# Kernel optimization log

Measured on AMD Instinct MI355X. Metric: run time of the kernel, lower is better.

## Reference

```python
import jax, jax.numpy as jnp
import numpy as np

N_HEADS = 16


def layernorm(x, g, b, eps=1e-5):
    mu = jnp.mean(x, axis=-1, keepdims=True)
    var = jnp.var(x, axis=-1, keepdims=True)
    return (x - mu) * jax.lax.rsqrt(var + eps) * g + b


def mha(x, w_qkv, b_qkv, w_o, b_o, n_heads):
    # standard multi-head self-attention (dropout off / eval mode)
    B, S, D = x.shape
    hd = D // n_heads
    qkv = x @ w_qkv + b_qkv                      # [B,S,3D]
    q, k, v = jnp.split(qkv, 3, axis=-1)
    q = q.reshape(B, S, n_heads, hd).transpose(0, 2, 1, 3)  # bhsd
    k = k.reshape(B, S, n_heads, hd).transpose(0, 2, 1, 3)
    v = v.reshape(B, S, n_heads, hd).transpose(0, 2, 1, 3)
    att = jnp.einsum('bhqd,bhkd->bhqk', q, k) / jnp.sqrt(jnp.asarray(hd, x.dtype))
    att = jax.nn.softmax(att, axis=-1)
    out = jnp.einsum('bhqk,bhkd->bhqd', att, v)
    out = out.transpose(0, 2, 1, 3).reshape(B, S, D)
    return out @ w_o + b_o


def setup_inputs() -> dict:
    key = jax.random.key(0)
    ks = jax.random.split(key, 12)
    B, Sx, Sz, D = 4, 1024, 1024, 1024
    H = D * 4
    s = 0.02
    return {
        'x': jax.random.normal(ks[0], (B, Sx, D), jnp.float32),
        'z': jax.random.normal(ks[1], (B, Sz, D), jnp.float32),
        'g1': jnp.ones((D,), jnp.float32),
        'b1': jnp.zeros((D,), jnp.float32),
        'w_qkv': jax.random.normal(ks[2], (D, 3 * D), jnp.float32) * s,
        'b_qkv': jnp.zeros((3 * D,), jnp.float32),
        'w_o': jax.random.normal(ks[3], (D, D), jnp.float32) * s,
        'b_o': jnp.zeros((D,), jnp.float32),
        'w_kv': jax.random.normal(ks[4], (D, 2 * D), jnp.float32) * s,
        'b_kv': jnp.zeros((2 * D,), jnp.float32),
        'g2': jnp.ones((D,), jnp.float32),
        'b2': jnp.zeros((D,), jnp.float32),
        'w_m1': jax.random.normal(ks[5], (D, H), jnp.float32) * s,
        'b_m1': jnp.zeros((H,), jnp.float32),
        'w_m2': jax.random.normal(ks[6], (H, D), jnp.float32) * s,
        'b_m2': jnp.zeros((D,), jnp.float32),
    }


def reference(x, z, g1, b1, w_qkv, b_qkv, w_o, b_o, w_kv, b_kv, g2, b2, w_m1, b_m1, w_m2, b_m2):
    # q = x + self_mha(ln1(x))
    q = x + mha(layernorm(x, g1, b1), w_qkv, b_qkv, w_o, b_o, N_HEADS)
    # single-head cross attention: k,v from z, scale by sqrt(dim)
    kv = z @ w_kv + b_kv
    k, v = jnp.split(kv, 2, axis=-1)            # each [B,Sz,D]
    scale = jnp.sqrt(jnp.asarray(k.shape[-1], x.dtype))
    att = jax.nn.softmax(jnp.einsum('bqd,bkd->bqk', q, k) / scale, axis=-1)
    out = jnp.einsum('bqk,bkd->bqd', att, v)
    # out = out + mlp(ln2(out))
    h = layernorm(out, g2, b2)
    h = jax.nn.gelu(h @ w_m1 + b_m1) @ w_m2 + b_m2
    return out + h
```

## Files before the change

kernel.cpp:

```cpp
#include <hip/hip_runtime.h>
#include <cstdint>
#include <cstddef>

using u16 = unsigned short;

typedef __attribute__((ext_vector_type(4))) float f32x4;
typedef __attribute__((ext_vector_type(8))) short bf16x8;

#define DEV static __device__ __forceinline__

DEV float bf2f(u16 v) {
  union { unsigned u; float f; } x; x.u = ((unsigned)v) << 16; return x.f;
}
DEV u16 f2bf(float f) {
  union { float f; unsigned u; } x; x.f = f;
  unsigned r = x.u + 0x7fffu + ((x.u >> 16) & 1u);
  return (u16)(r >> 16);
}
DEV void gload16(const void* g, void* l) {
  __builtin_amdgcn_global_load_lds((const __attribute__((address_space(1))) void*)g,
                                   (__attribute__((address_space(3))) void*)l, 16, 0, 0);
}
DEV float fast_gelu(float x) {
  float y = 0.7978845608028654f * (x + 0.044715f * x * x * x);
  y = fminf(fmaxf(y, -15.0f), 15.0f);
  float e = __expf(2.0f * y);
  float t = (e - 1.0f) / (e + 1.0f);
  return 0.5f * x * (1.0f + t);
}

template <typename OutT, bool GELU, int BN, bool SPLIT>
__global__ __launch_bounds__(256, 2) void gemm_nt(
    const u16* __restrict__ A, const u16* __restrict__ Bt, OutT* __restrict__ C,
    int K, int lda, int ldb, int ldc,
    const float* __restrict__ bias,
    const float* __restrict__ resF, const u16* __restrict__ resB, int ldr,
    float scale,
    long long sA, long long sB, long long sC, long long sR,
    int kSlices)
{
  constexpr int NW = (BN == 128) ? 64 : 32;
  constexpr int NJ = NW / 16;
  __shared__ u16 As[128 * 32];
  __shared__ u16 Bs[BN * 32];

  const int z = blockIdx.z;
  const int bz = z / kSlices;
  const int ks = z - bz * kSlices;
  const int Ksl = K / kSlices;
  const int kbeg = ks * Ksl, kend = kbeg + Ksl;

  A  += (size_t)bz * sA;
  Bt += (size_t)bz * sB;
  if constexpr (SPLIT) C += (size_t)ks * sC;
  else                 C += (size_t)bz * sC;
  const int m0 = blockIdx.y * 128, n0 = blockIdx.x * BN;
  const int tid = threadIdx.x;
  const int lane = tid & 63, wave = tid >> 6;
  const int wm = (wave >> 1) * 64, wn = (wave & 1) * NW;
  const int m15 = lane & 15, quad = lane >> 4;

  const u16* Ab = A + (size_t)m0 * lda;
  const u16* Bb = Bt + (size_t)n0 * ldb;
  const int r0 = tid >> 2, cc8 = (tid & 3) * 8;

  f32x4 acc[4][NJ];
#pragma unroll
  for (int i = 0; i < 4; i++)
#pragma unroll
    for (int j = 0; j < NJ; j++) acc[i][j] = (f32x4){0.f, 0.f, 0.f, 0.f};

  for (int k0 = kbeg; k0 < kend; k0 += 32) {
    __syncthreads();
    gload16(Ab + (size_t)r0 * lda + k0 + cc8,        &As[tid * 8]);
    gload16(Ab + (size_t)(r0 + 64) * lda + k0 + cc8, &As[2048 + tid * 8]);
    gload16(Bb + (size_t)r0 * ldb + k0 + cc8,        &Bs[tid * 8]);
    if constexpr (BN == 128)
      gload16(Bb + (size_t)(r0 + 64) * ldb + k0 + cc8, &Bs[2048 + tid * 8]);
    __syncthreads();
    bf16x8 af[4], bfr[NJ];
#pragma unroll
    for (int i = 0; i < 4; i++) af[i]  = *(const bf16x8*)&As[(wm + i * 16 + m15) * 32 + quad * 8];
#pragma unroll
    for (int j = 0; j < NJ; j++) bfr[j] = *(const bf16x8*)&Bs[(wn + j * 16 + m15) * 32 + quad * 8];
#pragma unroll
    for (int i = 0; i < 4; i++)
#pragma unroll
      for (int j = 0; j < NJ; j++)
        acc[i][j] = __builtin_amdgcn_mfma_f32_16x16x32_bf16(af[i], bfr[j], acc[i][j], 0, 0, 0);
  }

  const float* resFb = resF ? resF + (size_t)bz * sR : nullptr;
  const u16*   resBb = resB ? resB + (size_t)bz * sR : nullptr;

#pragma unroll
  for (int i = 0; i < 4; i++) {
    const int rowb = m0 + wm + i * 16 + quad * 4;
#pragma unroll
    for (int r = 0; r < 4; r++) {
      const size_t rowoff = (size_t)(rowb + r) * ldc;
      const size_t resoff = (size_t)(rowb + r) * ldr;
#pragma unroll
      for (int j = 0; j < NJ; j++) {
        const int col = n0 + wn + j * 16 + m15;
        float v = acc[i][j][r] * scale;
        if constexpr (SPLIT) {
          ((u16*)C)[rowoff + col] = f2bf(v);
        } else {
          if (bias) v += bias[col];
          if (GELU) v = fast_gelu(v);
          if (resFb) v += resFb[resoff + col];
          if (resBb) v += bf2f(resBb[resoff + col]);
          if constexpr (sizeof(OutT) == 4) C[rowoff + col] = v;
          else ((u16*)C)[rowoff + col] = f2bf(v);
        }
      }
    }
  }
}

__global__ __launch_bounds__(256) void mlp2_reduce_k(
    const u16* __restrict__ part, long long sliceStride,
    const u16* __restrict__ outb, const float* __restrict__ b_m2,
    float* __restrict__ outF)
{
  const size_t i = (size_t)blockIdx.x * 256 + threadIdx.x;
  const int col = (int)((i * 4) & 1023);
  const ushort4 u = ((const ushort4*)outb)[i];
  float4 o;
  o.x = bf2f(u.x) + b_m2[col + 0];
  o.y = bf2f(u.y) + b_m2[col + 1];
  o.z = bf2f(u.z) + b_m2[col + 2];
  o.w = bf2f(u.w) + b_m2[col + 3];
#pragma unroll
  for (int ks = 0; ks < 4; ks++) {
    const ushort4 p = ((const ushort4*)(part + (size_t)ks * sliceStride))[i];
    o.x += bf2f(p.x); o.y += bf2f(p.y); o.z += bf2f(p.z); o.w += bf2f(p.w);
  }
  ((float4*)outF)[i] = o;
}

__global__ __launch_bounds__(256) void transpose_all_k(
    const float* __restrict__ w_qkv, const float* __restrict__ w_o,
    const float* __restrict__ w_kv,  const float* __restrict__ w_m1,
    const float* __restrict__ w_m2,
    u16* __restrict__ wqkvT, u16* __restrict__ woT, u16* __restrict__ wkvT,
    u16* __restrict__ wm1T,  u16* __restrict__ wm2T)
{
  __shared__ u16 tile[32][33];
  int idx = blockIdx.x;
  const float* in; u16* out; int gx, ldin, ldout;
  if (idx < 3072)      { in = w_qkv; out = wqkvT; gx = 96;  ldin = 3072; ldout = 1024; }
  else if (idx < 4096) { idx -= 3072; in = w_o;  out = woT;  gx = 32;  ldin = 1024; ldout = 1024; }
  else if (idx < 6144) { idx -= 4096; in = w_kv; out = wkvT; gx = 64;  ldin = 2048; ldout = 1024; }
  else if (idx < 10240){ idx -= 6144; in = w_m1; out = wm1T; gx = 128; ldin = 4096; ldout = 1024; }
  else                 { idx -= 10240; in = w_m2; out = wm2T; gx = 32; ldin = 1024; ldout = 4096; }
  const int bx = idx % gx, by = idx / gx;
  const int tx = threadIdx.x & 31, ty = threadIdx.x >> 5;
  const int x = bx * 32 + tx;
#pragma unroll
  for (int j = 0; j < 4; j++)
    tile[ty + j * 8][tx] = f2bf(in[(size_t)(by * 32 + ty + j * 8) * ldin + x]);
  __syncthreads();
  const int x2 = by * 32 + tx;
#pragma unroll
  for (int j = 0; j < 4; j++)
    out[(size_t)(bx * 32 + ty + j * 8) * ldout + x2] = tile[tx][ty + j * 8];
}

__global__ __launch_bounds__(256) void transpose_v_self(
    const u16* __restrict__ qkv, u16* __restrict__ vT)
{
  __shared__ u16 tile[32][33];
  const int z = blockIdx.z, b = z >> 4, h = z & 15;
  const u16* in = qkv + (size_t)b * 1024 * 3072 + 2048 + h * 64;
  u16* out = vT + (size_t)z * 64 * 1024;
  const int tx = threadIdx.x & 31, ty = threadIdx.x >> 5;
  const int key0 = blockIdx.x * 32, d0 = blockIdx.y * 32;
#pragma unroll
  for (int j = 0; j < 4; j++)
    tile[ty + j * 8][tx] = in[(size_t)(key0 + ty + j * 8) * 3072 + d0 + tx];
  __syncthreads();
#pragma unroll
  for (int j = 0; j < 4; j++)
    out[(size_t)(d0 + ty + j * 8) * 1024 + key0 + tx] = tile[tx][ty + j * 8];
}

__global__ __launch_bounds__(256, 2) void flash_self_attn2(
    const u16* __restrict__ qkv, const u16* __restrict__ vT, u16* __restrict__ outp)
{
  __shared__ u16 Ks[64 * 72];
  __shared__ u16 Vs[64 * 72];
  __shared__ u16 Ps[128 * 72];
  const int b = blockIdx.z, h = blockIdx.y, q0 = blockIdx.x * 128;
  const int tid = threadIdx.x;
  const int lane = tid & 63, w = tid >> 6;
  const int m15 = lane & 15, quad = lane >> 4;

  const size_t base = (size_t)b * 1024 * 3072;
  const u16* qb  = qkv + base + (size_t)q0 * 3072 + h * 64;
  const u16* kb  = qkv + base + 1024 + h * 64;
  const u16* vtb = vT + (size_t)(b * 16 + h) * 64 * 1024;

  const int r8 = tid >> 3, c8 = (tid & 7) * 8;

  bf16x8 aq[2][2];
#pragma unroll
  for (int rb = 0; rb < 2; rb++)
#pragma unroll
    for (int kk = 0; kk < 2; kk++)
      aq[rb][kk] = *(const bf16x8*)(qb + (size_t)(w * 32 + rb * 16 + m15) * 3072 + kk * 32 + quad * 8);

  float m_i[2][4], l_i[2][4];
  f32x4 oacc[2][4];
#pragma unroll
  for (int rb = 0; rb < 2; rb++) {
#pragma unroll
    for (int r = 0; r < 4; r++) { m_i[rb][r] = -1e30f; l_i[rb][r] = 0.f; }
#pragma unroll
    for (int d = 0; d < 4; d++) oacc[rb][d] = (f32x4){0.f, 0.f, 0.f, 0.f};
  }

  for (int kt = 0; kt < 16; kt++) {
    const int key0 = kt * 64;
    bf16x8 kreg[2], vreg[2];
#pragma unroll
    for (int i = 0; i < 2; i++) {
      kreg[i] = *(const bf16x8*)(kb + (size_t)(key0 + r8 + i * 32) * 3072 + c8);
      vreg[i] = *(const bf16x8*)(vtb + (size_t)(r8 + i * 32) * 1024 + key0 + c8);
    }
    __syncthreads();
#pragma unroll
    for (int i = 0; i < 2; i++) {
      *(bf16x8*)&Ks[(r8 + i * 32) * 72 + c8] = kreg[i];
      *(bf16x8*)&Vs[(r8 + i * 32) * 72 + c8] = vreg[i];
    }
    __syncthreads();

    f32x4 sacc[2][4];
#pragma unroll
    for (int rb = 0; rb < 2; rb++)
#pragma unroll
      for (int n = 0; n < 4; n++) sacc[rb][n] = (f32x4){0.f, 0.f, 0.f, 0.f};
#pragma unroll
    for (int kk = 0; kk < 2; kk++)
#pragma unroll
      for (int n = 0; n < 4; n++) {
        const bf16x8 bk = *(const bf16x8*)&Ks[(n * 16 + m15) * 72 + kk * 32 + quad * 8];
#pragma unroll
        for (int rb = 0; rb < 2; rb++)
          sacc[rb][n] = __builtin_amdgcn_mfma_f32_16x16x32_bf16(aq[rb][kk], bk, sacc[rb][n], 0, 0, 0);
      }

#pragma unroll
    for (int rb = 0; rb < 2; rb++) {
      float al[4], rs[4];
#pragma unroll
      for (int r = 0; r < 4; r++) {
        float v = fmaxf(fmaxf(sacc[rb][0][r], sacc[rb][1][r]), fmaxf(sacc[rb][2][r], sacc[rb][3][r]));
        v *= 0.125f;
#pragma unroll
        for (int off = 1; off < 16; off <<= 1) v = fmaxf(v, __shfl_xor(v, off));
        const float mnew = fmaxf(m_i[rb][r], v);
        al[r] = __expf(m_i[rb][r] - mnew);
        m_i[rb][r] = mnew;
        rs[r] = 0.f;
      }
#pragma unroll
      for (int n = 0; n < 4; n++)
#pragma unroll
        for (int r = 0; r < 4; r++) {
          const float p = __expf(sacc[rb][n][r] * 0.125f - m_i[rb][r]);
          rs[r] += p;
          Ps[(w * 32 + rb * 16 + quad * 4 + r) * 72 + n * 16 + m15] = f2bf(p);
        }
#pragma unroll
      for (int r = 0; r < 4; r++) {
#pragma unroll
        for (int off = 1; off < 16; off <<= 1) rs[r] += __shfl_xor(rs[r], off);
        l_i[rb][r] = l_i[rb][r] * al[r] + rs[r];
      }
#pragma unroll
      for (int d = 0; d < 4; d++)
#pragma unroll
        for (int r = 0; r < 4; r++) oacc[rb][d][r] *= al[r];
    }

    bf16x8 ap[2][2];
#pragma unroll
    for (int rb = 0; rb < 2; rb++)
#pragma unroll
      for (int kk = 0; kk < 2; kk++)
        ap[rb][kk] = *(const bf16x8*)&Ps[(w * 32 + rb * 16 + m15) * 72 + kk * 32 + quad * 8];
#pragma unroll
    for (int kk = 0; kk < 2; kk++)
#pragma unroll
      for (int d = 0; d < 4; d++) {
        const bf16x8 bv = *(const bf16x8*)&Vs[(d * 16 + m15) * 72 + kk * 32 + quad * 8];
#pragma unroll
        for (int rb = 0; rb < 2; rb++)
          oacc[rb][d] = __builtin_amdgcn_mfma_f32_16x16x32_bf16(ap[rb][kk], bv, oacc[rb][d], 0, 0, 0);
      }
  }

#pragma unroll
  for (int rb = 0; rb < 2; rb++) {
    u16* ob = outp + (size_t)(b * 1024 + q0 + w * 32 + rb * 16 + quad * 4) * 1024 + h * 64 + m15;
#pragma unroll
    for (int r = 0; r < 4; r++) {
      const float inv = 1.0f / l_i[rb][r];
#pragma unroll
      for (int d = 0; d < 4; d++)
        ob[(size_t)r * 1024 + d * 16] = f2bf(oacc[rb][d][r] * inv);
    }
  }
}

template <typename TIn>
__global__ __launch_bounds__(256) void layernorm_k(
    const TIn* __restrict__ x, const float* __restrict__ g, const float* __restrict__ bb,
    u16* __restrict__ y)
{
  const int row = blockIdx.x;
  const int t = threadIdx.x;
  float v[4];
  if constexpr (sizeof(TIn) == 4) {
    const float4 f = ((const float4*)((const float*)x + (size_t)row * 1024))[t];
    v[0] = f.x; v[1] = f.y; v[2] = f.z; v[3] = f.w;
  } else {
    const ushort4 u = ((const ushort4*)((const u16*)x + (size_t)row * 1024))[t];
    v[0] = bf2f(u.x); v[1] = bf2f(u.y); v[2] = bf2f(u.z); v[3] = bf2f(u.w);
  }
  float s = v[0] + v[1] + v[2] + v[3];
  float sq = v[0]*v[0] + v[1]*v[1] + v[2]*v[2] + v[3]*v[3];
#pragma unroll
  for (int off = 1; off < 64; off <<= 1) { s += __shfl_xor(s, off); sq += __shfl_xor(sq, off); }
  __shared__ float red[8];
  const int wv = t >> 6;
  if ((t & 63) == 0) { red[wv] = s; red[4 + wv] = sq; }
  __syncthreads();
  s = red[0] + red[1] + red[2] + red[3];
  sq = red[4] + red[5] + red[6] + red[7];
  const float mean = s * (1.0f / 1024.0f);
  const float var = sq * (1.0f / 1024.0f) - mean * mean;
  const float rstd = rsqrtf(var + 1e-5f);
  const int c = t * 4;
  ushort4 o;
  o.x = f2bf((v[0] - mean) * rstd * g[c + 0] + bb[c + 0]);
  o.y = f2bf((v[1] - mean) * rstd * g[c + 1] + bb[c + 1]);
  o.z = f2bf((v[2] - mean) * rstd * g[c + 2] + bb[c + 2]);
  o.w = f2bf((v[3] - mean) * rstd * g[c + 3] + bb[c + 3]);
  ((ushort4*)(y + (size_t)row * 1024))[t] = o;
}

__global__ __launch_bounds__(256) void softmax_rows_k(const float* __restrict__ S, u16* __restrict__ P)
{
  const int row = blockIdx.x;
  const int t = threadIdx.x;
  const float4 f = ((const float4*)(S + (size_t)row * 1024))[t];
  float mx = fmaxf(fmaxf(f.x, f.y), fmaxf(f.z, f.w));
#pragma unroll
  for (int off = 1; off < 64; off <<= 1) mx = fmaxf(mx, __shfl_xor(mx, off));
  __shared__ float red[8];
  const int wv = t >> 6;
  if ((t & 63) == 0) red[wv] = mx;
  __syncthreads();
  mx = fmaxf(fmaxf(red[0], red[1]), fmaxf(red[2], red[3]));
  float e0 = __expf(f.x - mx), e1 = __expf(f.y - mx), e2 = __expf(f.z - mx), e3 = __expf(f.w - mx);
  float s = e0 + e1 + e2 + e3;
#pragma unroll
  for (int off = 1; off < 64; off <<= 1) s += __shfl_xor(s, off);
  if ((t & 63) == 0) red[4 + wv] = s;
  __syncthreads();
  s = red[4] + red[5] + red[6] + red[7];
  const float inv = 1.0f / s;
  ushort4 o; o.x = f2bf(e0 * inv); o.y = f2bf(e1 * inv); o.z = f2bf(e2 * inv); o.w = f2bf(e3 * inv);
  ((ushort4*)(P + (size_t)row * 1024))[t] = o;
}

__global__ __launch_bounds__(256) void transpose_k(
    const u16* __restrict__ in, u16* __restrict__ out,
    int ldin, int ldout, long long sIn, long long sOut)
{
  __shared__ u16 tile[32][33];
  in  += (size_t)blockIdx.z * sIn;
  out += (size_t)blockIdx.z * sOut;
  const int tx = threadIdx.x & 31, ty = threadIdx.x >> 5;
  const int x = blockIdx.x * 32 + tx;
#pragma unroll
  for (int j = 0; j < 4; j++)
    tile[ty + j * 8][tx] = in[(size_t)(blockIdx.y * 32 + ty + j * 8) * ldin + x];
  __syncthreads();
  const int x2 = blockIdx.y * 32 + tx;
#pragma unroll
  for (int j = 0; j < 4; j++)
    out[(size_t)(blockIdx.x * 32 + ty + j * 8) * ldout + x2] = tile[tx][ty + j * 8];
}

__global__ __launch_bounds__(256) void cast_f2b_k(const float* __restrict__ in, u16* __restrict__ out)
{
  const size_t i = (size_t)blockIdx.x * 256 + threadIdx.x;
  const float4 f = ((const float4*)in)[i];
  ushort4 o; o.x = f2bf(f.x); o.y = f2bf(f.y); o.z = f2bf(f.z); o.w = f2bf(f.w);
  ((ushort4*)out)[i] = o;
}

extern "C" void kernel_launch(void* const* d_in, const int* in_sizes, int n_in,
                              void* d_out, int out_size, void* d_ws, size_t ws_size,
                              hipStream_t stream)
{
  const float* x     = (const float*)d_in[0];
  const float* z     = (const float*)d_in[1];
  const float* g1    = (const float*)d_in[2];
  const float* b1    = (const float*)d_in[3];
  const float* w_qkv = (const float*)d_in[4];
  const float* b_qkv = (const float*)d_in[5];
  const float* w_o   = (const float*)d_in[6];
  const float* b_o   = (const float*)d_in[7];
  const float* w_kv  = (const float*)d_in[8];
  const float* b_kv  = (const float*)d_in[9];
  const float* g2    = (const float*)d_in[10];
  const float* b2    = (const float*)d_in[11];
  const float* w_m1  = (const float*)d_in[12];
  const float* b_m1  = (const float*)d_in[13];
  const float* w_m2  = (const float*)d_in[14];
  const float* b_m2  = (const float*)d_in[15];
  float* outF = (float*)d_out;

  char* ws = (char*)d_ws;
  const size_t MB = 1024ull * 1024ull;
  u16*   qkv   = (u16*)(ws + 0);
  u16*   Pm    = (u16*)(ws + 0);
  u16*   hm    = (u16*)(ws + 0);
  u16*   zb    = (u16*)(ws + 24 * MB);
  u16*   vTs   = (u16*)(ws + 24 * MB);
  u16*   xln   = (u16*)(ws + 32 * MB);
  u16*   mpart = (u16*)(ws + 32 * MB);
  u16*   qbuf  = (u16*)(ws + 40 * MB);
  u16*   kv    = (u16*)(ws + 48 * MB);
  float* Ssc   = (float*)(ws + 64 * MB);
  u16*   h1    = (u16*)(ws + 64 * MB);
  u16*   outb  = (u16*)(ws + 80 * MB);
  u16*   wqkvT = (u16*)(ws + 88 * MB);
  u16*   woT   = (u16*)(ws + 94 * MB);
  u16*   wkvT  = (u16*)(ws + 96 * MB);
  u16*   wm1T  = (u16*)(ws + 100 * MB);
  u16*   wm2T  = (u16*)(ws + 108 * MB);
  u16*   vT    = (u16*)(ws + 116 * MB);

  dim3 blk(256);
  const long long M1 = 1024 * 1024;

  hipLaunchKernelGGL(transpose_all_k, dim3(14336), blk, 0, stream,
                     w_qkv, w_o, w_kv, w_m1, w_m2, wqkvT, woT, wkvT, wm1T, wm2T);

  hipLaunchKernelGGL(cast_f2b_k, dim3(4096), blk, 0, stream, z, zb);
  hipLaunchKernelGGL((layernorm_k<float>), dim3(4096), blk, 0, stream, x, g1, b1, xln);

  hipLaunchKernelGGL((gemm_nt<u16, false, 128, false>), dim3(16, 32, 1), blk, 0, stream,
                     zb, wkvT, kv, 1024, 1024, 1024, 2048,
                     b_kv, (const float*)nullptr, (const u16*)nullptr, 0, 1.0f, 0LL, 0LL, 0LL, 0LL, 1);
  hipLaunchKernelGGL((gemm_nt<u16, false, 128, false>), dim3(24, 32, 1), blk, 0, stream,
                     xln, wqkvT, qkv, 1024, 1024, 1024, 3072,
                     b_qkv, (const float*)nullptr, (const u16*)nullptr, 0, 1.0f, 0LL, 0LL, 0LL, 0LL, 1);
  hipLaunchKernelGGL(transpose_v_self, dim3(32, 2, 64), blk, 0, stream, qkv, vTs);
  hipLaunchKernelGGL(flash_self_attn2, dim3(8, 16, 4), blk, 0, stream, qkv, vTs, xln);
  hipLaunchKernelGGL((gemm_nt<u16, false, 64, false>), dim3(16, 32, 1), blk, 0, stream,
                     xln, woT, qbuf, 1024, 1024, 1024, 1024,
                     b_o, x, (const u16*)nullptr, 1024, 1.0f, 0LL, 0LL, 0LL, 0LL, 1);
  hipLaunchKernelGGL((gemm_nt<float, false, 64, false>), dim3(16, 8, 4), blk, 0, stream,
                     qbuf, kv, Ssc, 1024, 1024, 2048, 1024,
                     (const float*)nullptr, (const float*)nullptr, (const u16*)nullptr, 0,
                     0.03125f, M1, 2 * M1, M1, 0LL, 1);
  hipLaunchKernelGGL(softmax_rows_k, dim3(4096), blk, 0, stream, Ssc, Pm);
  hipLaunchKernelGGL(transpose_k, dim3(32, 32, 4), blk, 0, stream,
                     kv + 1024, vT, 2048, 1024, 2 * M1, M1);
  hipLaunchKernelGGL((gemm_nt<u16, false, 64, false>), dim3(16, 8, 4), blk, 0, stream,
                     Pm, vT, outb, 1024, 1024, 1024, 1024,
                     (const float*)nullptr, (const float*)nullptr, (const u16*)nullptr, 0,
                     1.0f, M1, M1, M1, 0LL, 1);
  hipLaunchKernelGGL((layernorm_k<u16>), dim3(4096), blk, 0, stream, (const u16*)outb, g2, b2, h1);
  hipLaunchKernelGGL((gemm_nt<u16, true, 128, false>), dim3(32, 32, 1), blk, 0, stream,
                     h1, wm1T, hm, 1024, 1024, 1024, 4096,
                     b_m1, (const float*)nullptr, (const u16*)nullptr, 0, 1.0f, 0LL, 0LL, 0LL, 0LL, 1);
  hipLaunchKernelGGL((gemm_nt<u16, false, 128, true>), dim3(8, 32, 4), blk, 0, stream,
                     hm, wm2T, mpart, 4096, 4096, 4096, 1024,
                     (const float*)nullptr, (const float*)nullptr, (const u16*)nullptr, 0,
                     1.0f, 0LL, 0LL, 4LL * M1, 0LL, 4);
  hipLaunchKernelGGL(mlp2_reduce_k, dim3(4096), blk, 0, stream,
                     mpart, 4LL * M1, outb, b_m2, outF);
}
```

Baseline: 520.0 us.

## Shrink self-attention query tile, fold scale into Q, use DPP and MFMA row sums

The flash self-attention kernel now processes 64 queries per block (16 per wave) instead of 128, doubling the grid and raising the launch-bounds occupancy hint to 5. The 1/8 scale is pre-applied to Q in bf16, exp is computed with exp2 and a log2(e) factor, and the row max uses DPP row-broadcast steps instead of shuffles. Row sums are taken with an MFMA against a ones vector on the bf16-rounded P, replacing shuffle reductions. Each block now loads K/V tiles for half as many queries, which doubles K/V traffic, and rounding Q after scaling adds a small precision change.

Result: faster. 499.8 us (-3.9%).

```diff
diff --git a/kernel.cpp b/kernel.cpp
--- a/kernel.cpp
+++ b/kernel.cpp
@@ -27,6 +27,16 @@
   float e = __expf(2.0f * y);
   float t = (e - 1.0f) / (e + 1.0f);
   return 0.5f * x * (1.0f + t);
+}
+
+DEV float rowmax16_dpp(float v) {
+  union { float f; int i; } a, b;
+  a.f = v;
+  b.i = __builtin_amdgcn_update_dpp(0, a.i, 0x121, 0xf, 0xf, true); a.f = fmaxf(a.f, b.f);
+  b.i = __builtin_amdgcn_update_dpp(0, a.i, 0x122, 0xf, 0xf, true); a.f = fmaxf(a.f, b.f);
+  b.i = __builtin_amdgcn_update_dpp(0, a.i, 0x124, 0xf, 0xf, true); a.f = fmaxf(a.f, b.f);
+  b.i = __builtin_amdgcn_update_dpp(0, a.i, 0x128, 0xf, 0xf, true); a.f = fmaxf(a.f, b.f);
+  return a.f;
 }
 
 template <typename OutT, bool GELU, int BN, bool SPLIT>
@@ -186,16 +196,17 @@
     out[(size_t)(d0 + ty + j * 8) * 1024 + key0 + tx] = tile[tx][ty + j * 8];
 }
 
-__global__ __launch_bounds__(256, 2) void flash_self_attn2(
+__global__ __launch_bounds__(256, 5) void flash_self_attn3(
     const u16* __restrict__ qkv, const u16* __restrict__ vT, u16* __restrict__ outp)
 {
   __shared__ u16 Ks[64 * 72];
   __shared__ u16 Vs[64 * 72];
-  __shared__ u16 Ps[128 * 72];
-  const int b = blockIdx.z, h = blockIdx.y, q0 = blockIdx.x * 128;
+  __shared__ u16 Ps[4][16 * 72];
+  const int b = blockIdx.z, h = blockIdx.y, q0 = blockIdx.x * 64;
   const int tid = threadIdx.x;
   const int lane = tid & 63, w = tid >> 6;
   const int m15 = lane & 15, quad = lane >> 4;
+  const float L2E = 1.4426950408889634f;
 
   const size_t base = (size_t)b * 1024 * 3072;
   const u16* qb  = qkv + base + (size_t)q0 * 3072 + h * 64;
@@ -204,22 +215,26 @@
 
   const int r8 = tid >> 3, c8 = (tid & 7) * 8;
 
-  bf16x8 aq[2][2];
-#pragma unroll
-  for (int rb = 0; rb < 2; rb++)
-#pragma unroll
-    for (int kk = 0; kk < 2; kk++)
-      aq[rb][kk] = *(const bf16x8*)(qb + (size_t)(w * 32 + rb * 16 + m15) * 3072 + kk * 32 + quad * 8);
-
-  float m_i[2][4], l_i[2][4];
-  f32x4 oacc[2][4];
-#pragma unroll
-  for (int rb = 0; rb < 2; rb++) {
-#pragma unroll
-    for (int r = 0; r < 4; r++) { m_i[rb][r] = -1e30f; l_i[rb][r] = 0.f; }
-#pragma unroll
-    for (int d = 0; d < 4; d++) oacc[rb][d] = (f32x4){0.f, 0.f, 0.f, 0.f};
-  }
+  bf16x8 aq[2];
+#pragma unroll
+  for (int kk = 0; kk < 2; kk++) {
+    const bf16x8 raw = *(const bf16x8*)(qb + (size_t)(w * 16 + m15) * 3072 + kk * 32 + quad * 8);
+#pragma unroll
+    for (int j = 0; j < 8; j++)
+      ((u16*)&aq[kk])[j] = f2bf(bf2f(((const u16*)&raw)[j]) * 0.125f);
+  }
+
+  const short oneb = (short)0x3F80;
+  const bf16x8 ones = {oneb, oneb, oneb, oneb, oneb, oneb, oneb, oneb};
+
+  float mL[4];
+  f32x4 lacc;
+  f32x4 oacc[4];
+#pragma unroll
+  for (int r = 0; r < 4; r++) mL[r] = -3.0e38f;
+  lacc = (f32x4){0.f, 0.f, 0.f, 0.f};
+#pragma unroll
+  for (int d = 0; d < 4; d++) oacc[d] = (f32x4){0.f, 0.f, 0.f, 0.f};
 
   for (int kt = 0; kt < 16; kt++) {
     const int key0 = kt * 64;
@@ -237,82 +252,61 @@
     }
     __syncthreads();
 
-    f32x4 sacc[2][4];
-#pragma unroll
-    for (int rb = 0; rb < 2; rb++)
-#pragma unroll
-      for (int n = 0; n < 4; n++) sacc[rb][n] = (f32x4){0.f, 0.f, 0.f, 0.f};
+    f32x4 sacc[4];
+#pragma unroll
+    for (int n = 0; n < 4; n++) sacc[n] = (f32x4){0.f, 0.f, 0.f, 0.f};
 #pragma unroll
     for (int kk = 0; kk < 2; kk++)
 #pragma unroll
       for (int n = 0; n < 4; n++) {
         const bf16x8 bk = *(const bf16x8*)&Ks[(n * 16 + m15) * 72 + kk * 32 + quad * 8];
-#pragma unroll
-        for (int rb = 0; rb < 2; rb++)
-          sacc[rb][n] = __builtin_amdgcn_mfma_f32_16x16x32_bf16(aq[rb][kk], bk, sacc[rb][n], 0, 0, 0);
+        sacc[n] = __builtin_amdgcn_mfma_f32_16x16x32_bf16(aq[kk], bk, sacc[n], 0, 0, 0);
       }
 
-#pragma unroll
-    for (int rb = 0; rb < 2; rb++) {
-      float al[4], rs[4];
+    float al[4];
+#pragma unroll
+    for (int r = 0; r < 4; r++) {
+      float v = fmaxf(fmaxf(sacc[0][r], sacc[1][r]), fmaxf(sacc[2][r], sacc[3][r]));
+      v = rowmax16_dpp(v) * L2E;
+      const float mnew = fmaxf(mL[r], v);
+      al[r] = __builtin_amdgcn_exp2f(mL[r] - mnew);
+      mL[r] = mnew;
+    }
+#pragma unroll
+    for (int n = 0; n < 4; n++)
 #pragma unroll
       for (int r = 0; r < 4; r++) {
-        float v = fmaxf(fmaxf(sacc[rb][0][r], sacc[rb][1][r]), fmaxf(sacc[rb][2][r], sacc[rb][3][r]));
-        v *= 0.125f;
-#pragma unroll
-        for (int off = 1; off < 16; off <<= 1) v = fmaxf(v, __shfl_xor(v, off));
-        const float mnew = fmaxf(m_i[rb][r], v);
-        al[r] = __expf(m_i[rb][r] - mnew);
-        m_i[rb][r] = mnew;
-        rs[r] = 0.f;
+        const float p = __builtin_amdgcn_exp2f(fmaf(sacc[n][r], L2E, -mL[r]));
+        Ps[w][(quad * 4 + r) * 72 + n * 16 + m15] = f2bf(p);
       }
 #pragma unroll
-      for (int n = 0; n < 4; n++)
-#pragma unroll
-        for (int r = 0; r < 4; r++) {
-          const float p = __expf(sacc[rb][n][r] * 0.125f - m_i[rb][r]);
-          rs[r] += p;
-          Ps[(w * 32 + rb * 16 + quad * 4 + r) * 72 + n * 16 + m15] = f2bf(p);
-        }
-#pragma unroll
-      for (int r = 0; r < 4; r++) {
-#pragma unroll
-        for (int off = 1; off < 16; off <<= 1) rs[r] += __shfl_xor(rs[r], off);
-        l_i[rb][r] = l_i[rb][r] * al[r] + rs[r];
-      }
-#pragma unroll
-      for (int d = 0; d < 4; d++)
-#pragma unroll
-        for (int r = 0; r < 4; r++) oacc[rb][d][r] *= al[r];
+    for (int r = 0; r < 4; r++) {
+      lacc[r] *= al[r];
+#pragma unroll
+      for (int d = 0; d < 4; d++) oacc[d][r] *= al[r];
     }
 
-    bf16x8 ap[2][2];
-#pragma unroll
-    for (int rb = 0; rb < 2; rb++)
-#pragma unroll
-      for (int kk = 0; kk < 2; kk++)
-        ap[rb][kk] = *(const bf16x8*)&Ps[(w * 32 + rb * 16 + m15) * 72 + kk * 32 + quad * 8];
+    bf16x8 ap[2];
+    ap[0] = *(const bf16x8*)&Ps[w][m15 * 72 + quad * 8];
+    ap[1] = *(const bf16x8*)&Ps[w][m15 * 72 + 32 + quad * 8];
+    lacc = __builtin_amdgcn_mfma_f32_16x16x32_bf16(ap[0], ones, lacc, 0, 0, 0);
+    lacc = __builtin_amdgcn_mfma_f32_16x16x32_bf16(ap[1], ones, lacc, 0, 0, 0);
 #pragma unroll
     for (int kk = 0; kk < 2; kk++)
 #pragma unroll
       for (int d = 0; d < 4; d++) {
         const bf16x8 bv = *(const bf16x8*)&Vs[(d * 16 + m15) * 72 + kk * 32 + quad * 8];
-#pragma unroll
-        for (int rb = 0; rb < 2; rb++)
-          oacc[rb][d] = __builtin_amdgcn_mfma_f32_16x16x32_bf16(ap[rb][kk], bv, oacc[rb][d], 0, 0, 0);
+        oacc[d] = __builtin_amdgcn_mfma_f32_16x16x32_bf16(ap[kk], bv, oacc[d], 0, 0, 0);
       }
   }
 
-#pragma unroll
-  for (int rb = 0; rb < 2; rb++) {
-    u16* ob = outp + (size_t)(b * 1024 + q0 + w * 32 + rb * 16 + quad * 4) * 1024 + h * 64 + m15;
-#pragma unroll
-    for (int r = 0; r < 4; r++) {
-      const float inv = 1.0f / l_i[rb][r];
-#pragma unroll
-      for (int d = 0; d < 4; d++)
-        ob[(size_t)r * 1024 + d * 16] = f2bf(oacc[rb][d][r] * inv);
-    }
+  u16* ob = outp + (size_t)(b * 1024 + q0 + w * 16 + quad * 4) * 1024 + h * 64 + m15;
+#pragma unroll
+  for (int r = 0; r < 4; r++) {
+    const float inv = 1.0f / lacc[r];
+#pragma unroll
+    for (int d = 0; d < 4; d++)
+      ob[(size_t)r * 1024 + d * 16] = f2bf(oacc[d][r] * inv);
   }
 }
 
@@ -464,7 +458,7 @@
                      xln, wqkvT, qkv, 1024, 1024, 1024, 3072,
                      b_qkv, (const float*)nullptr, (const u16*)nullptr, 0, 1.0f, 0LL, 0LL, 0LL, 0LL, 1);
   hipLaunchKernelGGL(transpose_v_self, dim3(32, 2, 64), blk, 0, stream, qkv, vTs);
-  hipLaunchKernelGGL(flash_self_attn2, dim3(8, 16, 4), blk, 0, stream, qkv, vTs, xln);
+  hipLaunchKernelGGL(flash_self_attn3, dim3(16, 16, 4), blk, 0, stream, qkv, vTs, xln);
   hipLaunchKernelGGL((gemm_nt<u16, false, 64, false>), dim3(16, 32, 1), blk, 0, stream,
                      xln, woT, qbuf, 1024, 1024, 1024, 1024,
                      b_o, x, (const u16*)nullptr, 1024, 1.0f, 0LL, 0LL, 0LL, 0LL, 1);
```
